# Kernel optimization log

Measured on AMD Instinct MI355X. Metric: run time of the kernel, lower is better.

Reference implementation:

```python
import jax, jax.numpy as jnp
import numpy as np

K = 8192  # particles
T = 4096  # timesteps
LOG2PI = float(np.log(2.0 * np.pi))


def _normal_logpdf(x, mu):
    # Normal(mu, 1).log_prob(x)
    return -0.5 * (x - mu) ** 2 - 0.5 * LOG2PI


def setup_inputs() -> dict:
    key = jax.random.key(0)
    k1, k2, k3, k4 = jax.random.split(key, 4)
    x = jax.random.normal(k1, (T,), dtype=jnp.float32)          # observations
    w0 = jax.random.normal(k2, (K,), dtype=jnp.float32)          # Pw=N(0,1) samples
    z = jax.random.normal(k3, (K, T), dtype=jnp.float32)         # Qz=N(0,1) samples
    u = jax.random.uniform(k4, (T, K), dtype=jnp.float32)        # resampling uniforms
    return {"x": x, "w0": w0, "z": z, "u": u}


def reference(x, w0, z, u):
    # Precompute terms that the torch code computes once before the loop.
    log_Qz = _normal_logpdf(z, 0.0)                 # [K, T]  q.Qz().log_prob(z)
    log_PxGz = _normal_logpdf(x[None, :], z)        # [K, T]  p.PxGz(z).log_prob(x)
    delta = log_PxGz - log_Qz                       # [K, T]
    logK = jnp.log(jnp.asarray(K, dtype=z.dtype))

    def step(w, inp):
        z_t, d_t, u_t = inp                         # each [K]
        # log_ws = p.PzGw(w).log_prob(z_t) + log_PxGz_t - log_Qz_t
        log_ws = _normal_logpdf(z_t, w) + d_t       # [K]
        lme = jax.nn.logsumexp(log_ws) - logK       # logmeanexp over particles
        # Categorical(logits=log_ws).sample([K]) via inverse-CDF with uniforms
        cdf = jnp.cumsum(jax.nn.softmax(log_ws))    # [K]
        idx = jnp.clip(jnp.searchsorted(cdf, u_t), 0, K - 1)  # [K]
        return w[idx], lme                          # resample: w = w[idx]

    _, res = jax.lax.scan(step, w0, (z.T, delta.T, u))  # scan over T timesteps
    return jnp.sum(res)
```

## Files before the change

### kernel.cpp

```cpp
#include <hip/hip_runtime.h>
#include <math.h>

#define KP 8192
#define TSTEPS 4096
#define BLOCK 1024
#define PT 8
#define NWAVES 16
#define NBUCK 8192

#define SW2(i) ((i) + ((i) >> 3))
#define CDF_PAD 9216

template <int CTRL, int RM>
__device__ __forceinline__ float dpp_add_f(float x) {
  int s = __builtin_amdgcn_update_dpp(0, __float_as_int(x), CTRL, RM, 0xF, false);
  return x + __int_as_float(s);
}
template <int CTRL, int RM>
__device__ __forceinline__ int dpp_max_i(int x) {
  int s = __builtin_amdgcn_update_dpp(0, x, CTRL, RM, 0xF, false);
  return x > s ? x : s;
}
__device__ __forceinline__ float wscan64_add(float x) {
  x = dpp_add_f<0x111, 0xF>(x); x = dpp_add_f<0x112, 0xF>(x);
  x = dpp_add_f<0x114, 0xF>(x); x = dpp_add_f<0x118, 0xF>(x);
  x = dpp_add_f<0x142, 0xA>(x); x = dpp_add_f<0x143, 0xC>(x);
  return x;
}
__device__ __forceinline__ int wscan64_max(int x) {
  x = dpp_max_i<0x111, 0xF>(x); x = dpp_max_i<0x112, 0xF>(x);
  x = dpp_max_i<0x114, 0xF>(x); x = dpp_max_i<0x118, 0xF>(x);
  x = dpp_max_i<0x142, 0xA>(x); x = dpp_max_i<0x143, 0xC>(x);
  return x;
}
__device__ __forceinline__ float rscan16_add(float x) {
  x = dpp_add_f<0x111, 0xF>(x); x = dpp_add_f<0x112, 0xF>(x);
  x = dpp_add_f<0x114, 0xF>(x); x = dpp_add_f<0x118, 0xF>(x);
  return x;
}
__device__ __forceinline__ int rscan16_max(int x) {
  x = dpp_max_i<0x111, 0xF>(x); x = dpp_max_i<0x112, 0xF>(x);
  x = dpp_max_i<0x114, 0xF>(x); x = dpp_max_i<0x118, 0xF>(x);
  return x;
}
__device__ __forceinline__ float readlane_f(float v, int l) {
  return __int_as_float(__builtin_amdgcn_readlane(__float_as_int(v), l));
}

__global__ void transpose_k(const float* __restrict__ in, float* __restrict__ out) {
  __shared__ float tile[32][33];
  const int c0 = blockIdx.x * 32;
  const int r0 = blockIdx.y * 32;
  const int tx = threadIdx.x;
  const int ty = threadIdx.y;
#pragma unroll
  for (int i = 0; i < 32; i += 8)
    tile[ty + i][tx] = in[(size_t)(r0 + ty + i) * TSTEPS + c0 + tx];
  __syncthreads();
#pragma unroll
  for (int i = 0; i < 32; i += 8)
    out[(size_t)(c0 + ty + i) * KP + r0 + tx] = tile[tx][ty + i];
}

template <bool ZTRANS>
__global__ __launch_bounds__(BLOCK) void smc_scan(const float* __restrict__ x,
                                                  const float* __restrict__ w0,
                                                  const float* __restrict__ zsrc,
                                                  const float* __restrict__ u,
                                                  float* __restrict__ out) {
  extern __shared__ float sm[];
  float* wbufA = sm;
  float* wbufB = sm + KP;
  float* cdf_s = sm + 2 * KP;
  float* red   = cdf_s + CDF_PAD;
  int*   redi  = (int*)(red + NWAVES);
  int*   bcI   = redi + NWAVES;
  int*   L_s   = bcI + 4;

  const int tid = threadIdx.x;
  const int lane = tid & 63;
  const int wid = tid >> 6;
  const int kbase = tid * PT;
  const int wbase = SW2(kbase);

  float* wcur = wbufA;
  float* wnxt = wbufB;

  for (int i = tid; i < NBUCK; i += BLOCK) L_s[i] = 0;
  if (tid == 0) L_s[NBUCK] = KP - 1;

  float wv[PT];
  {
    float4 a = *(const float4*)(w0 + kbase);
    float4 b = *(const float4*)(w0 + kbase + 4);
    wv[0] = a.x; wv[1] = a.y; wv[2] = a.z; wv[3] = a.w;
    wv[4] = b.x; wv[5] = b.y; wv[6] = b.z; wv[7] = b.w;
    *(float4*)(wcur + kbase) = a;
    *(float4*)(wcur + kbase + 4) = b;
  }
  __syncthreads();

  float zn[PT], un[PT];
  float xt_next = x[0];
  if (ZTRANS) {
    float4 a = *(const float4*)(zsrc + kbase);
    float4 b = *(const float4*)(zsrc + kbase + 4);
    zn[0] = a.x; zn[1] = a.y; zn[2] = a.z; zn[3] = a.w;
    zn[4] = b.x; zn[5] = b.y; zn[6] = b.z; zn[7] = b.w;
  } else {
#pragma unroll
    for (int j = 0; j < PT; ++j) zn[j] = zsrc[(size_t)(kbase + j) * TSTEPS];
  }
  {
    float4 a = *(const float4*)(u + kbase);
    float4 b = *(const float4*)(u + kbase + 4);
    un[0] = a.x; un[1] = a.y; un[2] = a.z; un[3] = a.w;
    un[4] = b.x; un[5] = b.y; un[6] = b.z; un[7] = b.w;
  }

  float acc = 0.f;

  for (int t = 0; t < TSTEPS; ++t) {
    float zv[PT], uv[PT];
#pragma unroll
    for (int j = 0; j < PT; ++j) { zv[j] = zn[j]; uv[j] = un[j]; }
    const float xt = xt_next;

    if (t + 1 < TSTEPS) {
      xt_next = x[t + 1];
      if (ZTRANS) {
        float4 a = *(const float4*)(zsrc + (size_t)(t + 1) * KP + kbase);
        float4 b = *(const float4*)(zsrc + (size_t)(t + 1) * KP + kbase + 4);
        zn[0] = a.x; zn[1] = a.y; zn[2] = a.z; zn[3] = a.w;
        zn[4] = b.x; zn[5] = b.y; zn[6] = b.z; zn[7] = b.w;
      } else {
#pragma unroll
        for (int j = 0; j < PT; ++j)
          zn[j] = zsrc[(size_t)(kbase + j) * TSTEPS + t + 1];
      }
      float4 a = *(const float4*)(u + (size_t)(t + 1) * KP + kbase);
      float4 b = *(const float4*)(u + (size_t)(t + 1) * KP + kbase + 4);
      un[0] = a.x; un[1] = a.y; un[2] = a.z; un[3] = a.w;
      un[4] = b.x; un[5] = b.y; un[6] = b.z; un[7] = b.w;
    }

    float s[PT];
    float run = 0.f;
#pragma unroll
    for (int j = 0; j < PT; ++j) {
      float d = zv[j] - wv[j];
      float lw = fmaf(xt, zv[j], -0.5f * d * d);
      run += __expf(lw);
      s[j] = run;
    }
    const float wincl = wscan64_add(run);
    const float wexcl = wincl - run;
    if (lane == 63) red[wid] = wincl;
    __syncthreads();

    float v16 = rscan16_add(red[lane & 15]);
    const float total = readlane_f(v16, 15);
    const float wpre = wid ? readlane_f(v16, wid - 1) : 0.f;
    const float base = wpre + wexcl;
    const float nbOverT = (float)NBUCK / total;

    float cv[PT];
#pragma unroll
    for (int j = 0; j < PT; ++j) {
      cv[j] = base + s[j];
      cdf_s[wbase + j] = cv[j];
    }
    if (tid == BLOCK - 1) bcI[0] = (int)(cv[PT - 1] * nbOverT);
    {
      int4 z4; z4.x = z4.y = z4.z = z4.w = 0;
      *(int4*)(L_s + kbase) = z4;
      *(int4*)(L_s + kbase + 4) = z4;
    }
    if (tid == 0)
      acc += __logf(total) - 9.0109133472792886f
             - 0.5f * (1.8378770664093453f + xt * xt);
    __syncthreads();

    {
      const float cprev = tid ? cdf_s[SW2(kbase - 1)] : 0.f;
      int flo = (int)(cprev * nbOverT);
#pragma unroll
      for (int j = 0; j < PT; ++j) {
        int fhi = (int)(cv[j] * nbOverT);
        if (fhi > NBUCK - 1) fhi = NBUCK - 1;
        if (fhi > flo) L_s[flo + 1] = kbase + j;
        flo = fhi;
      }
    }
    __syncthreads();

    int4 ra = *(const int4*)(L_s + kbase);
    int4 rb = *(const int4*)(L_s + kbase + 4);
    int c0 = ra.x;
    int c1 = max(c0, ra.y);
    int c2 = max(c1, ra.z);
    int c3 = max(c2, ra.w);
    int c4 = max(c3, rb.x);
    int c5 = max(c4, rb.y);
    int c6 = max(c5, rb.z);
    int c7 = max(c6, rb.w);
    const int mincl = wscan64_max(c7);
    int mexcl = __shfl_up(mincl, 1);
    if (lane == 0) mexcl = 0;
    if (lane == 63) redi[wid] = mincl;
    __syncthreads();

    {
      int mv = rscan16_max(redi[lane & 15]);
      const int crosspre = wid ? __builtin_amdgcn_readlane(mv, wid - 1) : 0;
      const int fhiLast = bcI[0];
      int m = max(crosspre, mexcl);
      int4 oa, ob;
      m = max(m, ra.x); oa.x = (kbase + 0 > fhiLast) ? (KP - 1) : m;
      m = max(m, ra.y); oa.y = (kbase + 1 > fhiLast) ? (KP - 1) : m;
      m = max(m, ra.z); oa.z = (kbase + 2 > fhiLast) ? (KP - 1) : m;
      m = max(m, ra.w); oa.w = (kbase + 3 > fhiLast) ? (KP - 1) : m;
      m = max(m, rb.x); ob.x = (kbase + 4 > fhiLast) ? (KP - 1) : m;
      m = max(m, rb.y); ob.y = (kbase + 5 > fhiLast) ? (KP - 1) : m;
      m = max(m, rb.z); ob.z = (kbase + 6 > fhiLast) ? (KP - 1) : m;
      m = max(m, rb.w); ob.w = (kbase + 7 > fhiLast) ? (KP - 1) : m;
      *(int4*)(L_s + kbase) = oa;
      *(int4*)(L_s + kbase + 4) = ob;
    }
    __syncthreads();

    int lo[PT], len[PT];
    float tg[PT];
    int anylen = 0;
#pragma unroll
    for (int j = 0; j < PT; ++j) {
      tg[j] = uv[j] * total;
      int b = (int)(tg[j] * nbOverT);
      if (b > NBUCK - 1) b = NBUCK - 1;
      const int i0 = L_s[b];
      const int i1 = L_s[b + 1];
      lo[j] = i0;
      len[j] = i1 - i0;
      anylen |= len[j];
    }
    while (anylen) {
      anylen = 0;
#pragma unroll
      for (int j = 0; j < PT; ++j) {
        const int half = len[j] >> 1;
        const float c = cdf_s[SW2(lo[j] + half)];
        const bool adv = (c < tg[j]);
        lo[j] = adv ? lo[j] + half + 1 : lo[j];
        len[j] = adv ? len[j] - half - 1 : half;
        anylen |= len[j];
      }
    }

    float nw[PT];
#pragma unroll
    for (int j = 0; j < PT; ++j) nw[j] = wcur[lo[j]];
    {
      float4 a, b;
      a.x = nw[0]; a.y = nw[1]; a.z = nw[2]; a.w = nw[3];
      b.x = nw[4]; b.y = nw[5]; b.z = nw[6]; b.w = nw[7];
      *(float4*)(wnxt + kbase) = a;
      *(float4*)(wnxt + kbase + 4) = b;
    }
#pragma unroll
    for (int j = 0; j < PT; ++j) wv[j] = nw[j];
    float* tmp = wcur; wcur = wnxt; wnxt = tmp;
  }

  if (tid == 0) out[0] = acc;
}

extern "C" void kernel_launch(void* const* d_in, const int* in_sizes, int n_in,
                              void* d_out, int out_size, void* d_ws, size_t ws_size,
                              hipStream_t stream) {
  const float* x = (const float*)d_in[0];
  const float* w0 = (const float*)d_in[1];
  const float* z = (const float*)d_in[2];
  const float* u = (const float*)d_in[3];
  float* out = (float*)d_out;

  const size_t zbytes = (size_t)KP * TSTEPS * sizeof(float);
  const size_t shmem =
      (size_t)(2 * KP + CDF_PAD + NWAVES + NWAVES + 4 + NBUCK + 1) * sizeof(float);

  if (ws_size >= zbytes) {
    float* zT = (float*)d_ws;
    transpose_k<<<dim3(TSTEPS / 32, KP / 32), dim3(32, 8), 0, stream>>>(z, zT);
    smc_scan<true><<<1, BLOCK, shmem, stream>>>(x, w0, zT, u, out);
  } else {
    smc_scan<false><<<1, BLOCK, shmem, stream>>>(x, w0, z, u, out);
  }
}
```

Baseline: 20.67 ms.

## Normalize CDF, drop swizzled layout, and interpolate first search probe within bucket

Normalizes the CDF by the total so bucket indices use a constant scale and targets become the raw uniforms, removing a per-step divide and multiply. Stores the CDF contiguously with float4 writes instead of the padded swizzle, and keeps a separate per-thread end array for the previous-element lookup. Adds an interpolation-search first probe inside each bucket to shorten the binary search. Dropping the swizzle may bring back LDS bank conflicts on the scattered search reads, and normalization can shift results slightly through rounding.

```diff
diff --git a/kernel.cpp b/kernel.cpp
--- a/kernel.cpp
+++ b/kernel.cpp
@@ -7,9 +7,8 @@
 #define PT 8
 #define NWAVES 16
 #define NBUCK 8192
-
-#define SW2(i) ((i) + ((i) >> 3))
-#define CDF_PAD 9216
+#define NBF 8192.0f
+#define INV_NB (1.0f / 8192.0f)
 
 template <int CTRL, int RM>
 __device__ __forceinline__ float dpp_add_f(float x) {
@@ -72,7 +71,8 @@
   float* wbufA = sm;
   float* wbufB = sm + KP;
   float* cdf_s = sm + 2 * KP;
-  float* red   = cdf_s + CDF_PAD;
+  float* cend  = cdf_s + KP;
+  float* red   = cend + BLOCK;
   int*   redi  = (int*)(red + NWAVES);
   int*   bcI   = redi + NWAVES;
   int*   L_s   = bcI + 4;
@@ -81,7 +81,6 @@
   const int lane = tid & 63;
   const int wid = tid >> 6;
   const int kbase = tid * PT;
-  const int wbase = SW2(kbase);
 
   float* wcur = wbufA;
   float* wnxt = wbufB;
@@ -162,15 +161,20 @@
     const float total = readlane_f(v16, 15);
     const float wpre = wid ? readlane_f(v16, wid - 1) : 0.f;
     const float base = wpre + wexcl;
-    const float nbOverT = (float)NBUCK / total;
-
-    float cv[PT];
-#pragma unroll
-    for (int j = 0; j < PT; ++j) {
-      cv[j] = base + s[j];
-      cdf_s[wbase + j] = cv[j];
-    }
-    if (tid == BLOCK - 1) bcI[0] = (int)(cv[PT - 1] * nbOverT);
+    const float invT = 1.0f / total;
+
+    float cvn[PT];
+#pragma unroll
+    for (int j = 0; j < PT; ++j) cvn[j] = (base + s[j]) * invT;
+    {
+      float4 a, b;
+      a.x = cvn[0]; a.y = cvn[1]; a.z = cvn[2]; a.w = cvn[3];
+      b.x = cvn[4]; b.y = cvn[5]; b.z = cvn[6]; b.w = cvn[7];
+      *(float4*)(cdf_s + kbase) = a;
+      *(float4*)(cdf_s + kbase + 4) = b;
+    }
+    cend[tid] = cvn[PT - 1];
+    if (tid == BLOCK - 1) bcI[0] = (int)(cvn[PT - 1] * NBF);
     {
       int4 z4; z4.x = z4.y = z4.z = z4.w = 0;
       *(int4*)(L_s + kbase) = z4;
@@ -182,11 +186,11 @@
     __syncthreads();
 
     {
-      const float cprev = tid ? cdf_s[SW2(kbase - 1)] : 0.f;
-      int flo = (int)(cprev * nbOverT);
+      const float cprev = tid ? cend[tid - 1] : 0.f;
+      int flo = (int)(cprev * NBF);
 #pragma unroll
       for (int j = 0; j < PT; ++j) {
-        int fhi = (int)(cv[j] * nbOverT);
+        int fhi = (int)(cvn[j] * NBF);
         if (fhi > NBUCK - 1) fhi = NBUCK - 1;
         if (fhi > flo) L_s[flo + 1] = kbase + j;
         flo = fhi;
@@ -196,8 +200,7 @@
 
     int4 ra = *(const int4*)(L_s + kbase);
     int4 rb = *(const int4*)(L_s + kbase + 4);
-    int c0 = ra.x;
-    int c1 = max(c0, ra.y);
+    int c1 = max(ra.x, ra.y);
     int c2 = max(c1, ra.z);
     int c3 = max(c2, ra.w);
     int c4 = max(c3, rb.x);
@@ -230,17 +233,29 @@
     __syncthreads();
 
     int lo[PT], len[PT];
-    float tg[PT];
-    int anylen = 0;
+    float tg[PT], fr0[PT];
 #pragma unroll
     for (int j = 0; j < PT; ++j) {
-      tg[j] = uv[j] * total;
-      int b = (int)(tg[j] * nbOverT);
-      if (b > NBUCK - 1) b = NBUCK - 1;
+      tg[j] = uv[j];
+      const float fb = uv[j] * NBF;
+      int b = (int)fb;
+      b = min(b, NBUCK - 1);
+      fr0[j] = fb - (float)b;
       const int i0 = L_s[b];
       const int i1 = L_s[b + 1];
       lo[j] = i0;
       len[j] = i1 - i0;
+    }
+    int anylen = 0;
+#pragma unroll
+    for (int j = 0; j < PT; ++j) {
+      int off = (int)(fr0[j] * (float)len[j]);
+      off = min(off, len[j] - 1);
+      off = max(off, 0);
+      const float c = cdf_s[lo[j] + off];
+      const bool adv = (c < tg[j]) & (len[j] > 0);
+      lo[j] = adv ? lo[j] + off + 1 : lo[j];
+      len[j] = adv ? len[j] - off - 1 : (len[j] > 0 ? off : 0);
       anylen |= len[j];
     }
     while (anylen) {
@@ -248,8 +263,8 @@
 #pragma unroll
       for (int j = 0; j < PT; ++j) {
         const int half = len[j] >> 1;
-        const float c = cdf_s[SW2(lo[j] + half)];
-        const bool adv = (c < tg[j]);
+        const float c = cdf_s[lo[j] + half];
+        const bool adv = (c < tg[j]) & (len[j] > 0);
         lo[j] = adv ? lo[j] + half + 1 : lo[j];
         len[j] = adv ? len[j] - half - 1 : half;
         anylen |= len[j];
@@ -285,7 +300,7 @@
 
   const size_t zbytes = (size_t)KP * TSTEPS * sizeof(float);
   const size_t shmem =
-      (size_t)(2 * KP + CDF_PAD + NWAVES + NWAVES + 4 + NBUCK + 1) * sizeof(float);
+      (size_t)(3 * KP + BLOCK + NWAVES + NWAVES + 4 + NBUCK + 1) * sizeof(float);
 
   if (ws_size >= zbytes) {
     float* zT = (float*)d_ws;
```

Measured after the change: 20.86 ms. About the same (+0.9%).
